# Kernel tuning notes

Measured on AMD Instinct MI355X. Metric: run time of the kernel, lower is better.

## Reference

```python
import jax, jax.numpy as jnp
import numpy as np

N_LEVELS = 8
BASE_RES = 512
FEAT = 16
N = 1_000_000


def setup_inputs() -> dict:
    key = jax.random.key(0)
    k1, k2, k3 = jax.random.split(key, 3)
    x = jax.random.uniform(k1, (N, 3), dtype=jnp.float32)  # coords in [0,1]^3
    level = jax.random.uniform(k2, (N, 1), dtype=jnp.float32) * (N_LEVELS - 1)
    # texture param: uniform(-0.01, 0.01) as in torch init
    texture = (jax.random.uniform(k3, (3, BASE_RES, BASE_RES, FEAT), dtype=jnp.float32) - 0.5) * 0.02
    return {"x": x, "level": level, "texture": texture}


def _build_mips(texture):
    """Box-filtered mip pyramid: level k has resolution BASE_RES >> k."""
    mips = [texture]
    for _ in range(N_LEVELS - 1):
        t = mips[-1]
        r = t.shape[1]
        t = t.reshape(3, r // 2, 2, r // 2, 2, FEAT).mean(axis=(2, 4))
        mips.append(t)
    return mips


def _bilinear(tex_l, uv):
    """tex_l: (3, r, r, F) [plane, v(row), u(col), feat]; uv: (3, N, 2) in [0,1]. Clamp boundary."""
    r = tex_l.shape[1]
    c = uv * r - 0.5                     # nvdiffrast texel-center convention
    i0f = jnp.floor(c)
    f = c - i0f                          # (3, N, 2) fractional part
    i0 = jnp.clip(i0f.astype(jnp.int32), 0, r - 1)
    i1 = jnp.clip(i0f.astype(jnp.int32) + 1, 0, r - 1)
    u0, v0 = i0[..., 0], i0[..., 1]
    u1, v1 = i1[..., 0], i1[..., 1]
    plane = jnp.arange(3)[:, None]       # (3, 1) broadcast against (3, N)
    t00 = tex_l[plane, v0, u0]           # (3, N, F)
    t01 = tex_l[plane, v0, u1]
    t10 = tex_l[plane, v1, u0]
    t11 = tex_l[plane, v1, u1]
    fu = f[..., 0][..., None]
    fv = f[..., 1][..., None]
    return (t00 * (1 - fu) + t01 * fu) * (1 - fv) + (t10 * (1 - fu) + t11 * fu) * fv


def reference(x, level, texture):
    n = x.shape[0]
    # plane decomposition: uv = (yz, xz, xy), last dim is (u, v)
    uv = jnp.stack([x[:, jnp.array([1, 2])],
                    x[:, jnp.array([0, 2])],
                    x[:, jnp.array([0, 1])]], axis=0)  # (3, N, 2)
    lev = jnp.clip(level[:, 0], 0.0, N_LEVELS - 1)     # (N,)
    l0f = jnp.floor(lev)
    frac = lev - l0f
    l0 = l0f.astype(jnp.int32)
    mips = _build_mips(texture)
    acc = jnp.zeros((3, n, FEAT), dtype=texture.dtype)
    for k in range(N_LEVELS):
        w = jnp.where(l0 == k, 1.0 - frac, 0.0) + jnp.where(l0 + 1 == k, frac, 0.0)  # (N,)
        acc = acc + _bilinear(mips[k], uv) * w[None, :, None]
    # (3, N, F) -> (N, 3, F) -> (N, 3F), matching permute(1,2,0,3).view(N, 3F)
    return acc.transpose(1, 0, 2).reshape(n, 3 * FEAT)
```

## Files before the change

kernel.cpp:

```cpp
#include <hip/hip_runtime.h>

#define NLEV 8
#define BASE 512
#define FEAT 16

typedef float f4v __attribute__((ext_vector_type(4)));

__host__ __device__ __forceinline__ long mip_off(int k) {
    return 4194304L - (4194304L >> (2 * k - 2));
}

__global__ __launch_bounds__(256) void ds_kernel(const float* __restrict__ src,
                                                 float* __restrict__ dst, int r2) {
    int idx = blockIdx.x * blockDim.x + threadIdx.x;
    int total = 3 * r2 * r2 * 4;
    if (idx >= total) return;
    int fg = idx & 3;
    int rest = idx >> 2;
    int u = rest % r2; rest /= r2;
    int v = rest % r2;
    int p = rest / r2;
    int rs = r2 * 2;
    const float4* s4 = (const float4*)src;
    long i00 = (((long)p * rs + 2 * v) * rs + 2 * u) * 4 + fg;
    long i01 = i00 + 4;
    long i10 = i00 + (long)rs * 4;
    long i11 = i10 + 4;
    float4 a = s4[i00], b = s4[i01], c = s4[i10], d = s4[i11];
    float4 o;
    o.x = (a.x + b.x + c.x + d.x) * 0.25f;
    o.y = (a.y + b.y + c.y + d.y) * 0.25f;
    o.z = (a.z + b.z + c.z + d.z) * 0.25f;
    o.w = (a.w + b.w + c.w + d.w) * 0.25f;
    float4* d4 = (float4*)dst;
    d4[(((long)p * r2 + v) * r2 + u) * 4 + fg] = o;
}

__global__ __launch_bounds__(256) void tm_sample8(const float* __restrict__ x,
                                                  const float* __restrict__ level,
                                                  const float* __restrict__ tex0,
                                                  const float* __restrict__ ws,
                                                  float* __restrict__ out, int n) {
    int t = blockIdx.x * blockDim.x + threadIdx.x;
    int i = t >> 3;
    if (i >= n) return;
    int fg = t & 3;
    int usel = (t >> 2) & 1;

    float px = x[3 * i + 0];
    float py = x[3 * i + 1];
    float pz = x[3 * i + 2];
    float lev = fminf(fmaxf(level[i], 0.0f), (float)(NLEV - 1));
    float l0f = floorf(lev);
    float frac = lev - l0f;
    int l0 = (int)l0f;
    int k1 = min(l0 + 1, NLEV - 1);

    float uu[3] = {py, px, px};
    float vv[3] = {pz, pz, py};

    const float* texs[2];
    texs[0] = (l0 == 0) ? tex0 : (ws + mip_off(l0));
    texs[1] = ws + mip_off(k1);
    int rr[2] = {BASE >> l0, BASE >> k1};

    float4 tv[2][3][2];
    float wu[2][3];
    float fvv[2][3];

#pragma unroll
    for (int s = 0; s < 2; ++s) {
        int r = rr[s];
        float rf = (float)r;
        const float4* t4 = (const float4*)texs[s];
#pragma unroll
        for (int p = 0; p < 3; ++p) {
            float cu = uu[p] * rf - 0.5f;
            float cv = vv[p] * rf - 0.5f;
            float fu0 = floorf(cu), fv0 = floorf(cv);
            float fu = cu - fu0, fv = cv - fv0;
            int iu0 = (int)fu0, iv0 = (int)fv0;
            int u0 = min(max(iu0, 0), r - 1);
            int u1 = min(max(iu0 + 1, 0), r - 1);
            int v0 = min(max(iv0, 0), r - 1);
            int v1 = min(max(iv0 + 1, 0), r - 1);
            int u = usel ? u1 : u0;
            wu[s][p] = usel ? fu : (1.0f - fu);
            fvv[s][p] = fv;
            long pb = (long)p * r * r;
            tv[s][p][0] = t4[(pb + (long)v0 * r + u) * 4 + fg];
            tv[s][p][1] = t4[(pb + (long)v1 * r + u) * 4 + fg];
        }
    }

    float lw[2] = {1.0f - frac, frac};
    float4 res[3];
#pragma unroll
    for (int p = 0; p < 3; ++p) {
        float ax = 0.f, ay = 0.f, az = 0.f, aw = 0.f;
#pragma unroll
        for (int s = 0; s < 2; ++s) {
            float w0 = (1.0f - fvv[s][p]) * wu[s][p] * lw[s];
            float w1 = fvv[s][p] * wu[s][p] * lw[s];
            ax += tv[s][p][0].x * w0 + tv[s][p][1].x * w1;
            ay += tv[s][p][0].y * w0 + tv[s][p][1].y * w1;
            az += tv[s][p][0].z * w0 + tv[s][p][1].z * w1;
            aw += tv[s][p][0].w * w0 + tv[s][p][1].w * w1;
        }
        ax += __shfl_xor(ax, 4, 64);
        ay += __shfl_xor(ay, 4, 64);
        az += __shfl_xor(az, 4, 64);
        aw += __shfl_xor(aw, 4, 64);
        res[p] = make_float4(ax, ay, az, aw);
    }

    f4v* o4 = (f4v*)out;
    long ob = (long)i * 12;
    if (usel == 0) {
        f4v r0 = {res[0].x, res[0].y, res[0].z, res[0].w};
        f4v r2 = {res[2].x, res[2].y, res[2].z, res[2].w};
        __builtin_nontemporal_store(r0, &o4[ob + 0 + fg]);
        __builtin_nontemporal_store(r2, &o4[ob + 8 + fg]);
    } else {
        f4v r1 = {res[1].x, res[1].y, res[1].z, res[1].w};
        __builtin_nontemporal_store(r1, &o4[ob + 4 + fg]);
    }
}

extern "C" void kernel_launch(void* const* d_in, const int* in_sizes, int n_in,
                              void* d_out, int out_size, void* d_ws, size_t ws_size,
                              hipStream_t stream) {
    const float* x     = (const float*)d_in[0];
    const float* level = (const float*)d_in[1];
    const float* tex   = (const float*)d_in[2];
    float* out = (float*)d_out;
    float* ws  = (float*)d_ws;
    int n = in_sizes[0] / 3;

    const float* src = tex;
    for (int k = 1; k < NLEV; ++k) {
        int r2 = BASE >> k;
        float* dst = ws + mip_off(k);
        int total = 3 * r2 * r2 * 4;
        int blocks = (total + 255) / 256;
        ds_kernel<<<blocks, 256, 0, stream>>>(src, dst, r2);
        src = dst;
    }

    long tt = (long)n * 8;
    int blocks = (int)((tt + 255) / 256);
    tm_sample8<<<blocks, 256, 0, stream>>>(x, level, tex, ws, out, n);
}
```

Before: 159.1 us.

## Store mip pyramid and texture in fp16, sample with four threads per point

```diff
diff --git a/kernel.cpp b/kernel.cpp
--- a/kernel.cpp
+++ b/kernel.cpp
@@ -1,51 +1,92 @@
 #include <hip/hip_runtime.h>
+#include <hip/hip_fp16.h>
 
 #define NLEV 8
 #define BASE 512
-#define FEAT 16
-
+
+typedef _Float16 h8 __attribute__((ext_vector_type(8)));
 typedef float f4v __attribute__((ext_vector_type(4)));
 
-__host__ __device__ __forceinline__ long mip_off(int k) {
+__host__ __device__ __forceinline__ long moff(int k) {
     return 4194304L - (4194304L >> (2 * k - 2));
 }
-
-__global__ __launch_bounds__(256) void ds_kernel(const float* __restrict__ src,
-                                                 float* __restrict__ dst, int r2) {
+#define MIPS_HALVES 4194048L
+#define L0_OFF      MIPS_HALVES
+#define L0_HALVES   12582912L
+#define WS_NEED_FULL ((L0_OFF + L0_HALVES) * 2)
+
+__global__ __launch_bounds__(256) void cvt0(const float* __restrict__ src,
+                                            _Float16* __restrict__ dst) {
+    long idx = (long)blockIdx.x * blockDim.x + threadIdx.x;
+    if (idx >= L0_HALVES / 8) return;
+    const f4v* s = (const f4v*)src;
+    f4v a = s[idx * 2], b = s[idx * 2 + 1];
+    h8 o;
+    o[0] = (_Float16)a[0]; o[1] = (_Float16)a[1]; o[2] = (_Float16)a[2]; o[3] = (_Float16)a[3];
+    o[4] = (_Float16)b[0]; o[5] = (_Float16)b[1]; o[6] = (_Float16)b[2]; o[7] = (_Float16)b[3];
+    ((h8*)dst)[idx] = o;
+}
+
+__global__ __launch_bounds__(256) void ds16_first(const float* __restrict__ src,
+                                                  _Float16* __restrict__ dst, int r2) {
     int idx = blockIdx.x * blockDim.x + threadIdx.x;
-    int total = 3 * r2 * r2 * 4;
+    int total = 3 * r2 * r2 * 2;
     if (idx >= total) return;
-    int fg = idx & 3;
-    int rest = idx >> 2;
+    int g = idx & 1;
+    int rest = idx >> 1;
     int u = rest % r2; rest /= r2;
     int v = rest % r2;
     int p = rest / r2;
     int rs = r2 * 2;
-    const float4* s4 = (const float4*)src;
-    long i00 = (((long)p * rs + 2 * v) * rs + 2 * u) * 4 + fg;
-    long i01 = i00 + 4;
-    long i10 = i00 + (long)rs * 4;
-    long i11 = i10 + 4;
-    float4 a = s4[i00], b = s4[i01], c = s4[i10], d = s4[i11];
-    float4 o;
-    o.x = (a.x + b.x + c.x + d.x) * 0.25f;
-    o.y = (a.y + b.y + c.y + d.y) * 0.25f;
-    o.z = (a.z + b.z + c.z + d.z) * 0.25f;
-    o.w = (a.w + b.w + c.w + d.w) * 0.25f;
-    float4* d4 = (float4*)dst;
-    d4[(((long)p * r2 + v) * r2 + u) * 4 + fg] = o;
-}
-
-__global__ __launch_bounds__(256) void tm_sample8(const float* __restrict__ x,
+    const f4v* s4 = (const f4v*)src;
+    long t00 = ((long)p * rs + 2 * v) * rs + 2 * u;
+    long t01 = t00 + 1, t10 = t00 + rs, t11 = t10 + 1;
+    f4v a0 = s4[t00 * 4 + g * 2], a1 = s4[t00 * 4 + g * 2 + 1];
+    f4v b0 = s4[t01 * 4 + g * 2], b1 = s4[t01 * 4 + g * 2 + 1];
+    f4v c0 = s4[t10 * 4 + g * 2], c1 = s4[t10 * 4 + g * 2 + 1];
+    f4v d0 = s4[t11 * 4 + g * 2], d1 = s4[t11 * 4 + g * 2 + 1];
+    h8 o;
+#pragma unroll
+    for (int j = 0; j < 4; ++j) {
+        o[j]     = (_Float16)((a0[j] + b0[j] + c0[j] + d0[j]) * 0.25f);
+        o[4 + j] = (_Float16)((a1[j] + b1[j] + c1[j] + d1[j]) * 0.25f);
+    }
+    ((h8*)dst)[idx] = o;
+}
+
+__global__ __launch_bounds__(256) void ds16(const _Float16* __restrict__ src,
+                                            _Float16* __restrict__ dst, int r2) {
+    int idx = blockIdx.x * blockDim.x + threadIdx.x;
+    int total = 3 * r2 * r2 * 2;
+    if (idx >= total) return;
+    int g = idx & 1;
+    int rest = idx >> 1;
+    int u = rest % r2; rest /= r2;
+    int v = rest % r2;
+    int p = rest / r2;
+    int rs = r2 * 2;
+    const h8* s8 = (const h8*)src;
+    long t00 = ((long)p * rs + 2 * v) * rs + 2 * u;
+    long t01 = t00 + 1, t10 = t00 + rs, t11 = t10 + 1;
+    h8 A = s8[t00 * 2 + g], B = s8[t01 * 2 + g], C = s8[t10 * 2 + g], D = s8[t11 * 2 + g];
+    h8 o;
+#pragma unroll
+    for (int j = 0; j < 8; ++j)
+        o[j] = (_Float16)(((float)A[j] + (float)B[j] + (float)C[j] + (float)D[j]) * 0.25f);
+    ((h8*)dst)[idx] = o;
+}
+
+template <bool L0F16>
+__global__ __launch_bounds__(256) void tm_sample4(const float* __restrict__ x,
                                                   const float* __restrict__ level,
                                                   const float* __restrict__ tex0,
-                                                  const float* __restrict__ ws,
+                                                  const _Float16* __restrict__ wsh,
                                                   float* __restrict__ out, int n) {
     int t = blockIdx.x * blockDim.x + threadIdx.x;
-    int i = t >> 3;
+    int i = t >> 2;
     if (i >= n) return;
-    int fg = t & 3;
-    int usel = (t >> 2) & 1;
+    int fg = t & 1;
+    int usel = (t >> 1) & 1;
 
     float px = x[3 * i + 0];
     float py = x[3 * i + 1];
@@ -58,13 +99,13 @@
 
     float uu[3] = {py, px, px};
     float vv[3] = {pz, pz, py};
-
-    const float* texs[2];
-    texs[0] = (l0 == 0) ? tex0 : (ws + mip_off(l0));
-    texs[1] = ws + mip_off(k1);
     int rr[2] = {BASE >> l0, BASE >> k1};
 
-    float4 tv[2][3][2];
+    const _Float16* texs[2];
+    texs[0] = (l0 == 0) ? (wsh + L0_OFF) : (wsh + moff(l0));
+    texs[1] = wsh + moff(k1);
+
+    h8 tvh[2][3][2];
     float wu[2][3];
     float fvv[2][3];
 
@@ -72,7 +113,8 @@
     for (int s = 0; s < 2; ++s) {
         int r = rr[s];
         float rf = (float)r;
-        const float4* t4 = (const float4*)texs[s];
+        const h8* t8 = (const h8*)texs[s];
+        bool f32path = (!L0F16) && (s == 0) && (l0 == 0);
 #pragma unroll
         for (int p = 0; p < 3; ++p) {
             float cu = uu[p] * rf - 0.5f;
@@ -88,42 +130,67 @@
             wu[s][p] = usel ? fu : (1.0f - fu);
             fvv[s][p] = fv;
             long pb = (long)p * r * r;
-            tv[s][p][0] = t4[(pb + (long)v0 * r + u) * 4 + fg];
-            tv[s][p][1] = t4[(pb + (long)v1 * r + u) * 4 + fg];
+            long ti0 = pb + (long)v0 * r + u;
+            long ti1 = pb + (long)v1 * r + u;
+            if (f32path) {
+                const f4v* t4 = (const f4v*)tex0;
+                f4v a = t4[ti0 * 4 + fg * 2], b = t4[ti0 * 4 + fg * 2 + 1];
+                f4v c = t4[ti1 * 4 + fg * 2], d = t4[ti1 * 4 + fg * 2 + 1];
+                h8 A, B;
+#pragma unroll
+                for (int j = 0; j < 4; ++j) {
+                    A[j] = (_Float16)a[j]; A[4 + j] = (_Float16)b[j];
+                    B[j] = (_Float16)c[j]; B[4 + j] = (_Float16)d[j];
+                }
+                tvh[s][p][0] = A;
+                tvh[s][p][1] = B;
+            } else {
+                tvh[s][p][0] = t8[ti0 * 2 + fg];
+                tvh[s][p][1] = t8[ti1 * 2 + fg];
+            }
         }
     }
 
     float lw[2] = {1.0f - frac, frac};
-    float4 res[3];
-#pragma unroll
-    for (int p = 0; p < 3; ++p) {
-        float ax = 0.f, ay = 0.f, az = 0.f, aw = 0.f;
-#pragma unroll
-        for (int s = 0; s < 2; ++s) {
+    float acc[3][8];
+#pragma unroll
+    for (int p = 0; p < 3; ++p)
+#pragma unroll
+        for (int j = 0; j < 8; ++j) acc[p][j] = 0.f;
+
+#pragma unroll
+    for (int s = 0; s < 2; ++s)
+#pragma unroll
+        for (int p = 0; p < 3; ++p) {
             float w0 = (1.0f - fvv[s][p]) * wu[s][p] * lw[s];
             float w1 = fvv[s][p] * wu[s][p] * lw[s];
-            ax += tv[s][p][0].x * w0 + tv[s][p][1].x * w1;
-            ay += tv[s][p][0].y * w0 + tv[s][p][1].y * w1;
-            az += tv[s][p][0].z * w0 + tv[s][p][1].z * w1;
-            aw += tv[s][p][0].w * w0 + tv[s][p][1].w * w1;
+#pragma unroll
+            for (int j = 0; j < 8; ++j)
+                acc[p][j] += (float)tvh[s][p][0][j] * w0 + (float)tvh[s][p][1][j] * w1;
         }
-        ax += __shfl_xor(ax, 4, 64);
-        ay += __shfl_xor(ay, 4, 64);
-        az += __shfl_xor(az, 4, 64);
-        aw += __shfl_xor(aw, 4, 64);
-        res[p] = make_float4(ax, ay, az, aw);
-    }
+
+#pragma unroll
+    for (int p = 0; p < 3; ++p)
+#pragma unroll
+        for (int j = 0; j < 8; ++j)
+            acc[p][j] += __shfl_xor(acc[p][j], 2, 64);
 
     f4v* o4 = (f4v*)out;
-    long ob = (long)i * 12;
+    long ob = (long)i * 12 + fg * 2;
     if (usel == 0) {
-        f4v r0 = {res[0].x, res[0].y, res[0].z, res[0].w};
-        f4v r2 = {res[2].x, res[2].y, res[2].z, res[2].w};
-        __builtin_nontemporal_store(r0, &o4[ob + 0 + fg]);
-        __builtin_nontemporal_store(r2, &o4[ob + 8 + fg]);
+        f4v r0 = {acc[0][0], acc[0][1], acc[0][2], acc[0][3]};
+        f4v r1 = {acc[0][4], acc[0][5], acc[0][6], acc[0][7]};
+        f4v r4 = {acc[2][0], acc[2][1], acc[2][2], acc[2][3]};
+        f4v r5 = {acc[2][4], acc[2][5], acc[2][6], acc[2][7]};
+        __builtin_nontemporal_store(r0, &o4[ob + 0]);
+        __builtin_nontemporal_store(r1, &o4[ob + 1]);
+        __builtin_nontemporal_store(r4, &o4[ob + 8]);
+        __builtin_nontemporal_store(r5, &o4[ob + 9]);
     } else {
-        f4v r1 = {res[1].x, res[1].y, res[1].z, res[1].w};
-        __builtin_nontemporal_store(r1, &o4[ob + 4 + fg]);
+        f4v r2 = {acc[1][0], acc[1][1], acc[1][2], acc[1][3]};
+        f4v r3 = {acc[1][4], acc[1][5], acc[1][6], acc[1][7]};
+        __builtin_nontemporal_store(r2, &o4[ob + 4]);
+        __builtin_nontemporal_store(r3, &o4[ob + 5]);
     }
 }
 
@@ -134,20 +201,30 @@
     const float* level = (const float*)d_in[1];
     const float* tex   = (const float*)d_in[2];
     float* out = (float*)d_out;
-    float* ws  = (float*)d_ws;
+    _Float16* wsh = (_Float16*)d_ws;
     int n = in_sizes[0] / 3;
 
-    const float* src = tex;
-    for (int k = 1; k < NLEV; ++k) {
+    bool full = ws_size >= (size_t)WS_NEED_FULL;
+
+    {
+        int r2 = BASE >> 1;
+        int total = 3 * r2 * r2 * 2;
+        ds16_first<<<(total + 255) / 256, 256, 0, stream>>>(tex, wsh + moff(1), r2);
+    }
+    for (int k = 2; k < NLEV; ++k) {
         int r2 = BASE >> k;
-        float* dst = ws + mip_off(k);
-        int total = 3 * r2 * r2 * 4;
-        int blocks = (total + 255) / 256;
-        ds_kernel<<<blocks, 256, 0, stream>>>(src, dst, r2);
-        src = dst;
-    }
-
-    long tt = (long)n * 8;
+        int total = 3 * r2 * r2 * 2;
+        ds16<<<(total + 255) / 256, 256, 0, stream>>>(wsh + moff(k - 1), wsh + moff(k), r2);
+    }
+    if (full) {
+        long tot = L0_HALVES / 8;
+        cvt0<<<(int)((tot + 255) / 256), 256, 0, stream>>>(tex, wsh + L0_OFF);
+    }
+
+    long tt = (long)n * 4;
     int blocks = (int)((tt + 255) / 256);
-    tm_sample8<<<blocks, 256, 0, stream>>>(x, level, tex, ws, out, n);
-}
+    if (full)
+        tm_sample4<true><<<blocks, 256, 0, stream>>>(x, level, tex, wsh, out, n);
+    else
+        tm_sample4<false><<<blocks, 256, 0, stream>>>(x, level, tex, wsh, out, n);
+}
```

After: 152.9 us. 3.9% less time.
